# Performance work log

Measured on AMD Instinct MI355X. Metric: run time of the kernel, lower is better.

## Reference

```python
import jax, jax.numpy as jnp
import numpy as np

E, K, CAP = 8, 2, 48
RD, NC = 64, 10
LOAD_PEN, MIN_USE, TEMP = 2.0, 0.05, 1.0


def _conv(x, w):
    return jax.lax.conv_general_dilated(x, w, (1, 1), 'SAME',
                                        dimension_numbers=('NCHW', 'OIHW', 'NCHW'))


def _bn(x, g, b):
    # eval-mode BatchNorm2d with running_mean=0, running_var=1, eps=1e-5
    s = g / np.float32(np.sqrt(1.0 + 1e-5))
    return x * s[:, None, None] + b[:, None, None]


def _maxpool2(x):
    return jax.lax.reduce_window(x, -jnp.inf, jax.lax.max,
                                 (1, 1, 2, 2), (1, 1, 2, 2), 'VALID')


def setup_inputs() -> dict:
    key = jax.random.key(0)
    ks = iter(jax.random.split(key, 40))
    n = lambda shape, s=0.1: jax.random.normal(next(ks), shape, jnp.float32) * s
    B = 256
    return dict(
        x=jax.random.normal(next(ks), (B, 3, 32, 32), jnp.float32),
        # routing trunk
        tw1=n((32, 3, 3, 3)), tg1=jnp.ones(32), tb1=jnp.zeros(32),
        tw2=n((32, 32, 3, 3)), tg2=jnp.ones(32), tb2=jnp.zeros(32),
        tfw=n((RD, 128)), tfb=jnp.zeros(RD),
        # gate MLP
        gw1=n((RD // 2, RD)), gb1=jnp.zeros(RD // 2),
        gw2=n((E, RD // 2)), gb2=jnp.zeros(E),
        # per-expert feature extractors (stacked over E)
        ew1=n((E, 32, 3, 3, 3)), eg1=jnp.ones((E, 32)), eb1=jnp.zeros((E, 32)),
        ew2=n((E, 64, 32, 3, 3)), eg2=jnp.ones((E, 64)), eb2=jnp.zeros((E, 64)),
        ew3=n((E, 128, 64, 3, 3)), eg3=jnp.ones((E, 128)), eb3=jnp.zeros((E, 128)),
        efw=n((E, 128, 128)), efb=jnp.zeros((E, 128)),
        # per-expert classifiers (stacked over E)
        cw1=n((E, 64, 128)), cb1=jnp.zeros((E, 64)),
        cw2=n((E, NC, 64)), cb2=jnp.zeros((E, NC)),
    )


def _forward(x, tw1, tg1, tb1, tw2, tg2, tb2, tfw, tfb, gw1, gb1, gw2, gb2,
             ew1, eg1, eb1, ew2, eg2, eb2, ew3, eg3, eb3, efw, efb,
             cw1, cb1, cw2, cb2):
    B = x.shape[0]
    # ---- routing trunk ----
    h = jax.nn.relu(_bn(_conv(x, tw1), tg1, tb1))
    h = jax.nn.relu(_bn(_conv(h, tw2), tg2, tb2))
    h = _maxpool2(h)                                   # [B,32,16,16]
    h = h.reshape(B, 32, 2, 8, 2, 8).mean((3, 5))      # AdaptiveAvgPool2d(2)
    rf = jax.nn.relu(h.reshape(B, 128) @ tfw.T + tfb)  # [B,RD]
    # ---- gate ----
    scores = (jax.nn.relu(rf @ gw1.T + gb1) @ gw2.T + gb2) / TEMP  # [B,E]
    usage = jnp.ones(E, jnp.float32) / E               # expert_usage_ema buffer
    boost = jnp.where(usage < MIN_USE, (MIN_USE - usage) * 10.0, 0.0)
    balanced = scores + boost[None] - LOAD_PEN * usage[None]
    # ---- capacity-constrained top-k routing (eval: sample_order = arange) ----
    _, tk = jax.lax.top_k(balanced, K)                 # [B,K] int32

    def step(loads, tki):
        lt = loads[tki]                                # [K] loads of this sample's top-k
        avail = lt < CAP
        idx = jnp.where(jnp.any(avail), jnp.argmax(avail), jnp.argmin(lt))
        chosen = tki[idx]
        return loads.at[chosen].add(1.0), chosen

    _, chosen = jax.lax.scan(step, jnp.zeros(E, jnp.float32), tk)
    D = jax.nn.one_hot(chosen, E, dtype=bool)          # [B,E] dispatch mask

    # ---- experts: run each expert on the full batch, zero out unassigned ----
    def expert(w1, g1, b1, w2, g2, b2, w3, g3, b3, fw, fb, c1w, c1b, c2w, c2b):
        h = _maxpool2(jax.nn.relu(_bn(_conv(x, w1), g1, b1)))   # [B,32,16,16]
        h = _maxpool2(jax.nn.relu(_bn(_conv(h, w2), g2, b2)))   # [B,64,8,8]
        h = jax.nn.relu(_bn(_conv(h, w3), g3, b3)).mean((2, 3)) # GAP -> [B,128]
        f = jax.nn.relu(h @ fw.T + fb)
        return jax.nn.relu(f @ c1w.T + c1b) @ c2w.T + c2b        # [B,NC]

    outs = jax.vmap(expert)(ew1, eg1, eb1, ew2, eg2, eb2, ew3, eg3, eb3,
                            efw, efb, cw1, cb1, cw2, cb2)        # [E,B,NC]
    expert_outputs = jnp.where(D.T[:, :, None], outs, 0.0).transpose(1, 0, 2)  # [B,E,NC]

    # ---- combine via softmax over dispatched scores ----
    masked = jnp.where(D, balanced, -jnp.inf)
    rw = jax.nn.softmax(masked, axis=1) * D
    rw = rw / (rw.sum(1, keepdims=True) + 1e-12)
    final = jnp.einsum('be,bec->bc', rw, expert_outputs)         # [B,NC]
    return final, balanced, D


def reference(x, tw1, tg1, tb1, tw2, tg2, tb2, tfw, tfb, gw1, gb1, gw2, gb2,
              ew1, eg1, eb1, ew2, eg2, eb2, ew3, eg3, eb3, efw, efb,
              cw1, cb1, cw2, cb2):
    return _forward(x, tw1, tg1, tb1, tw2, tg2, tb2, tfw, tfb,
                    gw1, gb1, gw2, gb2, ew1, eg1, eb1, ew2, eg2, eb2,
                    ew3, eg3, eb3, efw, efb, cw1, cb1, cw2, cb2)
```

## Files before the change

### kernel.cpp

```cpp
#include <hip/hip_runtime.h>
#include <hip/hip_bf16.h>
#include <math.h>


#define BN_RS (1.0f / sqrtf(1.00001f))

typedef __attribute__((ext_vector_type(8))) short short8;
typedef __attribute__((ext_vector_type(4))) float floatx4;

static __device__ __forceinline__ ushort f2bf(float f) {
  unsigned u = __float_as_uint(f);
  unsigned r = (u + 0x7fffu + ((u >> 16) & 1u)) >> 16;
  return (ushort)r;
}
static __device__ __forceinline__ float bf2f(ushort h) {
  return __uint_as_float((unsigned)h << 16);
}

#define WS_TFP    0
#define WS_TK     262144
#define WS_W2H    264192
#define WS_W2L    282624
#define WS_EW2B   301056
#define WS_EW3B   595968

__global__ __launch_bounds__(256) void prep_kernel(
    const float* __restrict__ tw2, const float* __restrict__ ew2,
    const float* __restrict__ ew3, ushort* __restrict__ w2h,
    ushort* __restrict__ w2l, ushort* __restrict__ ew2b,
    ushort* __restrict__ ew3b)
{
  const int j = blockIdx.x * 256 + threadIdx.x;
  if (j < 9216) {
    int tap = j >> 10, oc = (j >> 5) & 31, ic = j & 31;
    float v = tw2[oc*288 + ic*9 + tap];
    ushort h = f2bf(v);
    w2h[j] = h;
    w2l[j] = f2bf(v - bf2f(h));
  } else if (j < 27648) {
    const int jj = (j - 9216) * 8;
    int e = jj / 18432, r2 = jj % 18432;
    int tap = r2 / 2048, r3 = r2 % 2048;
    int oc = r3 / 32, ic0 = r3 % 32;
    const float* src = &ew2[e*18432 + oc*288 + ic0*9 + tap];
    short8 o;
    #pragma unroll
    for (int k = 0; k < 8; ++k) o[k] = (short)f2bf(src[k*9]);
    *(short8*)&ew2b[jj] = o;
  } else if (j < 101376) {
    const int jj = (j - 27648) * 8;
    int e = jj / 73728, r2 = jj % 73728;
    int tap = r2 / 8192, r3 = r2 % 8192;
    int oc = r3 / 64, ic0 = r3 % 64;
    const float* src = &ew3[e*73728 + oc*576 + ic0*9 + tap];
    short8 o;
    #pragma unroll
    for (int k = 0; k < 8; ++k) o[k] = (short)f2bf(src[k*9]);
    *(short8*)&ew3b[jj] = o;
  }
}

__global__ __launch_bounds__(256) void trunk_kernel(
    const float* __restrict__ x, const float* __restrict__ tw1,
    const float* __restrict__ tg1, const float* __restrict__ tb1,
    const ushort* __restrict__ w2h, const ushort* __restrict__ w2l,
    const float* __restrict__ tg2, const float* __restrict__ tb2,
    float* __restrict__ tfp)
{
  __shared__ __align__(16) ushort smu[17696];
  float* smf = (float*)&smu[14400];
  const int t = threadIdx.x, blk = blockIdx.x;
  const int b = blk >> 3, rs = (blk >> 1) & 3, ch = blk & 1;
  const int r0 = rs * 8, c0 = ch * 16;

  {
    uint4 z = {0, 0, 0, 0};
    for (int j = t; j < 1800; j += 256) ((uint4*)smu)[j] = z;
  }
  for (int j = t; j < 720; j += 256) {
    int ic = j / 240, rem = j % 240, rr = rem / 20, c = rem % 20;
    int gy = r0 - 2 + rr, gx = c0 - 2 + c;
    float v = 0.f;
    if (gy >= 0 && gy < 32 && gx >= 0 && gx < 32)
      v = x[b*3072 + ic*1024 + gy*32 + gx];
    smf[j] = v;
  }
  for (int j = t; j < 864; j += 256) {
    int oc = j / 27, r = j % 27, ic = r / 9, k = r % 9;
    smf[720 + ic*288 + k*32 + oc] = tw1[j];
  }
  if (t < 32) { smf[1584 + t] = tg1[t]*BN_RS; smf[1584 + 32 + t] = tb1[t]; }
  __syncthreads();

  for (int it = 0; it < 2; ++it) {
    const int item = it*256 + t;
    if (item < 320) {
      const int oc = item & 31, rr = item >> 5;
      const int grow = r0 - 1 + rr;
      if (grow >= 0 && grow < 32) {
        float acc[18];
        #pragma unroll
        for (int c = 0; c < 18; ++c) acc[c] = 0.f;
        #pragma unroll 1
        for (int ic = 0; ic < 3; ++ic) {
          #pragma unroll 1
          for (int ky = 0; ky < 3; ++ky) {
            float wk[3];
            #pragma unroll
            for (int kx = 0; kx < 3; ++kx)
              wk[kx] = smf[720 + ic*288 + (ky*3 + kx)*32 + oc];
            const float* srow = &smf[ic*240 + (rr + ky)*20];
            float v[20];
            #pragma unroll
            for (int j4 = 0; j4 < 5; ++j4) {
              float4 q = *(const float4*)&srow[4*j4];
              v[4*j4] = q.x; v[4*j4+1] = q.y; v[4*j4+2] = q.z; v[4*j4+3] = q.w;
            }
            #pragma unroll
            for (int kx = 0; kx < 3; ++kx)
              #pragma unroll
              for (int c = 0; c < 18; ++c)
                acc[c] = fmaf(wk[kx], v[c+kx], acc[c]);
          }
        }
        const float s = smf[1584 + oc], bo = smf[1584 + 32 + oc];
        #pragma unroll
        for (int c = 0; c < 18; ++c) {
          const int gcol = c0 - 1 + c;
          float va = 0.f;
          if (gcol >= 0 && gcol < 32)
            va = fmaxf(fmaf(acc[c], s, bo), 0.f);
          ushort h = f2bf(va);
          ushort lo = f2bf(va - bf2f(h));
          const int ui = (rr*18 + c)*40 + oc;
          smu[ui] = h;
          smu[7200 + ui] = lo;
        }
      }
    }
  }
  __syncthreads();

  const int w4 = t >> 6, l = t & 63, col = l & 15, quad = l >> 4;
  const int nt = w4 & 1, yh = w4 >> 1;
  floatx4 acc2[4];
  #pragma unroll
  for (int y = 0; y < 4; ++y)
    #pragma unroll
    for (int i = 0; i < 4; ++i) acc2[y][i] = 0.f;

  #pragma unroll
  for (int dx = 0; dx < 3; ++dx) {
    #pragma unroll
    for (int dy = 0; dy < 3; ++dy) {
      const int wi = (dy*3 + dx)*1024 + (nt*16 + col)*32 + quad*8;
      short8 bh = *(const short8*)&w2h[wi];
      short8 bl = *(const short8*)&w2l[wi];
      #pragma unroll
      for (int y = 0; y < 4; ++y) {
        const int idx = ((yh*4 + y + dy)*18 + col + dx)*40 + quad*8;
        short8 ah = *(const short8*)&smu[idx];
        short8 al = *(const short8*)&smu[7200 + idx];
        acc2[y] = __builtin_amdgcn_mfma_f32_16x16x32_bf16(ah, bh, acc2[y], 0, 0, 0);
        acc2[y] = __builtin_amdgcn_mfma_f32_16x16x32_bf16(ah, bl, acc2[y], 0, 0, 0);
        acc2[y] = __builtin_amdgcn_mfma_f32_16x16x32_bf16(al, bh, acc2[y], 0, 0, 0);
      }
    }
  }

  {
    const int oc = nt*16 + col;
    const float s2 = tg2[oc]*BN_RS, bo2 = tb2[oc];
    float psum = 0.f;
    #pragma unroll
    for (int yp = 0; yp < 2; ++yp)
      #pragma unroll
      for (int i2 = 0; i2 < 2; ++i2) {
        float v00 = fmaxf(fmaf(acc2[2*yp][2*i2],     s2, bo2), 0.f);
        float v01 = fmaxf(fmaf(acc2[2*yp][2*i2+1],   s2, bo2), 0.f);
        float v10 = fmaxf(fmaf(acc2[2*yp+1][2*i2],   s2, bo2), 0.f);
        float v11 = fmaxf(fmaf(acc2[2*yp+1][2*i2+1], s2, bo2), 0.f);
        psum += fmaxf(fmaxf(v00, v01), fmaxf(v10, v11));
      }
    psum += __shfl_xor(psum, 16);
    psum += __shfl_xor(psum, 32);
    if (yh == 1 && quad == 0) smf[nt*32 + col] = psum;
    __syncthreads();
    if (yh == 0 && quad == 0) {
      float tot = psum + smf[nt*32 + col];
      tfp[b*256 + (rs*2 + ch)*32 + oc] = tot;
    }
  }
}

__global__ __launch_bounds__(64) void gate_kernel(
    const float* __restrict__ tfp, const float* __restrict__ tfw, const float* __restrict__ tfb,
    const float* __restrict__ gw1, const float* __restrict__ gb1,
    const float* __restrict__ gw2, const float* __restrict__ gb2,
    float* __restrict__ outBal, int* __restrict__ tk)
{
  __shared__ float feat[128], rf[64], g1[32], bal[8];
  const int b = blockIdx.x, t = threadIdx.x;
  #pragma unroll
  for (int h = 0; h < 2; ++h) {
    const int f = t + 64*h;
    const int oc = f >> 2, qy = (f >> 1) & 1, qx = f & 1;
    feat[f] = (tfp[b*256 + (4*qy + qx)*32 + oc] +
               tfp[b*256 + (4*qy + 2 + qx)*32 + oc]) * (1.f/64.f);
  }
  __syncthreads();
  {
    float a = tfb[t];
    const float4* wp = (const float4*)&tfw[t*128];
    #pragma unroll 8
    for (int i4 = 0; i4 < 32; ++i4) {
      float4 wv = wp[i4];
      a = fmaf(wv.x, feat[4*i4], a);   a = fmaf(wv.y, feat[4*i4+1], a);
      a = fmaf(wv.z, feat[4*i4+2], a); a = fmaf(wv.w, feat[4*i4+3], a);
    }
    rf[t] = fmaxf(a, 0.f);
  }
  __syncthreads();
  if (t < 32) {
    float a = gb1[t];
    const float4* wp = (const float4*)&gw1[t*64];
    #pragma unroll
    for (int i4 = 0; i4 < 16; ++i4) {
      float4 wv = wp[i4];
      a = fmaf(wv.x, rf[4*i4], a);   a = fmaf(wv.y, rf[4*i4+1], a);
      a = fmaf(wv.z, rf[4*i4+2], a); a = fmaf(wv.w, rf[4*i4+3], a);
    }
    g1[t] = fmaxf(a, 0.f);
  }
  __syncthreads();
  if (t < 8) {
    float a = gb2[t];
    const float4* wp = (const float4*)&gw2[t*32];
    #pragma unroll
    for (int i4 = 0; i4 < 8; ++i4) {
      float4 wv = wp[i4];
      a = fmaf(wv.x, g1[4*i4], a);   a = fmaf(wv.y, g1[4*i4+1], a);
      a = fmaf(wv.z, g1[4*i4+2], a); a = fmaf(wv.w, g1[4*i4+3], a);
    }
    const float v = a - 0.25f;
    bal[t] = v;
    outBal[b*8 + t] = v;
  }
  __syncthreads();
  if (t == 0) {
    int t0 = 0; float b0 = bal[0];
    #pragma unroll
    for (int e2 = 1; e2 < 8; ++e2) if (bal[e2] > b0) { b0 = bal[e2]; t0 = e2; }
    int t1 = -1; float b1 = -3.4e38f;
    #pragma unroll
    for (int e2 = 0; e2 < 8; ++e2) if (e2 != t0 && bal[e2] > b1) { b1 = bal[e2]; t1 = e2; }
    tk[b*2] = t0; tk[b*2 + 1] = t1;
  }
}

#define XA_IMG  0
#define XA_FEAT 3600
#define XA_SFF  3728
#define XA_SGG  3856
#define XA_XF   9040
#define XA_W1F  12508
#define XA_BN1F 13372
#define XA_SC   9040
__global__ __launch_bounds__(512, 2) void expALL_kernel(
    const float* __restrict__ x, const int* __restrict__ tk,
    const float* __restrict__ ew1, const float* __restrict__ eg1,
    const float* __restrict__ eb1, const ushort* __restrict__ ew2b,
    const float* __restrict__ eg2, const float* __restrict__ eb2,
    const ushort* __restrict__ ew3b, const float* __restrict__ eg3,
    const float* __restrict__ eb3, const float* __restrict__ efw,
    const float* __restrict__ efb, const float* __restrict__ cw1,
    const float* __restrict__ cb1, const float* __restrict__ cw2,
    const float* __restrict__ cb2, float* __restrict__ outF,
    float* __restrict__ outD)
{
  __shared__ __align__(16) ushort smu[27296];
  __shared__ int stk[512];
  __shared__ int sch;
  float* smf = (float*)smu;
  const int t = threadIdx.x, b = blockIdx.x;
  const int w8 = t >> 6, l = t & 63;
  const int col = l & 15, quad = l >> 4;

  stk[t] = tk[t];
  __syncthreads();
  if (t == 0) {
    unsigned long long Lp = 0ull;
    int chv = 0;
    for (int i = 0; i <= b; ++i) {
      const int a = stk[2*i], c = stk[2*i+1];
      const int la = (int)((Lp >> (a*8)) & 0xFFull);
      const int lc = (int)((Lp >> (c*8)) & 0xFFull);
      chv = (la < 48) ? a : ((lc < 48) ? c : ((la <= lc) ? a : c));
      Lp += 1ull << (chv*8);
    }
    sch = chv;
  } else {
    uint4 z; z.x = 0; z.y = 0; z.z = 0; z.w = 0;
    for (int j = t-1; j < 1620; j += 511) ((uint4*)smu)[j] = z;
    for (int j = t-1; j < 3468; j += 511) {
      int ic = j / 1156, rem = j % 1156, p = rem / 34, cpd = rem % 34;
      int gy = p - 1, gx = cpd - 1;
      float v = 0.f;
      if (gy >= 0 && gy < 32 && gx >= 0 && gx < 32) v = x[b*3072 + ic*1024 + gy*32 + gx];
      smf[XA_XF + j] = v;
    }
  }
  __syncthreads();
  const int e = sch;
  if (t < 8) outD[b*8 + t] = (t == e) ? 1.f : 0.f;

  const int ntile = w8 & 3, mhalf = w8 >> 2;
  short8 w2f[9];
  {
    const int oc2 = ntile*16 + col;
    #pragma unroll
    for (int tap = 0; tap < 9; ++tap)
      w2f[tap] = *(const short8*)&ew2b[(e*9 + tap)*2048 + oc2*32 + quad*8];
  }

  for (int j = t; j < 864; j += 512) {
    int oc = j / 27, r = j % 27, ic = r / 9, k = r % 9;
    smf[XA_W1F + ic*288 + k*32 + oc] = ew1[e*864 + j];
  }
  if (t < 32) { smf[XA_BN1F + t] = eg1[e*32 + t]*BN_RS; smf[XA_BN1F + 32 + t] = eb1[e*32 + t]; }
  __syncthreads();

  {
    const int g = t >> 5, c = t & 31;
    for (int rs = 0; rs < 4; ++rs) {
      const int r0 = rs * 8;
      float acc[2][8];
      #pragma unroll
      for (int o = 0; o < 2; ++o)
        #pragma unroll
        for (int r = 0; r < 8; ++r) acc[o][r] = 0.f;
      for (int ic = 0; ic < 3; ++ic) {
        float w[2][9];
        #pragma unroll
        for (int k = 0; k < 9; ++k) {
          float2 wv = *(const float2*)&smf[XA_W1F + ic*288 + k*32 + 2*g];
          w[0][k] = wv.x; w[1][k] = wv.y;
        }
        const float* src = &smf[XA_XF + ic*1156 + r0*34 + c];
        #pragma unroll
        for (int rr = 0; rr < 10; ++rr) {
          const float i0 = src[rr*34], i1 = src[rr*34 + 1], i2 = src[rr*34 + 2];
          #pragma unroll
          for (int dr = 0; dr < 3; ++dr) {
            const int r = rr - dr;
            if (r < 0 || r > 7) continue;
            #pragma unroll
            for (int o = 0; o < 2; ++o) {
              acc[o][r] = fmaf(w[o][dr*3+0], i0, acc[o][r]);
              acc[o][r] = fmaf(w[o][dr*3+1], i1, acc[o][r]);
              acc[o][r] = fmaf(w[o][dr*3+2], i2, acc[o][r]);
            }
          }
        }
      }
      #pragma unroll
      for (int o = 0; o < 2; ++o) {
        const int oc = 2*g + o;
        const float s = smf[XA_BN1F + oc], bo = smf[XA_BN1F + 32 + oc];
        float m[4];
        #pragma unroll
        for (int pr = 0; pr < 4; ++pr) {
          float v0 = fmaxf(fmaf(acc[o][2*pr],   s, bo), 0.f);
          float v1 = fmaxf(fmaf(acc[o][2*pr+1], s, bo), 0.f);
          m[pr] = fmaxf(v0, v1);
        }
        #pragma unroll
        for (int pr = 0; pr < 4; ++pr) {
          float nb = __shfl_xor(m[pr], 1);
          m[pr] = fmaxf(m[pr], nb);
        }
        if (!(c & 1)) {
          const int pc = c >> 1;
          #pragma unroll
          for (int pr = 0; pr < 4; ++pr)
            smu[XA_IMG + ((rs*4 + pr + 1)*18 + (pc + 1))*40 + oc] = f2bf(m[pr]);
        }
      }
    }
  }
  __syncthreads();

  const int oc3 = w8*16 + col;
  short8 w3f[9][2];
  #pragma unroll
  for (int tap = 0; tap < 9; ++tap)
    #pragma unroll
    for (int ks = 0; ks < 2; ++ks)
      w3f[tap][ks] = *(const short8*)&ew3b[(e*9 + tap)*8192 + oc3*64 + ks*32 + quad*8];

  {
    floatx4 acc[8];
    #pragma unroll
    for (int mt = 0; mt < 8; ++mt)
      #pragma unroll
      for (int i = 0; i < 4; ++i) acc[mt][i] = 0.f;

    #pragma unroll
    for (int tap = 0; tap < 9; ++tap) {
      const int dy = tap / 3, dx = tap % 3;
      #pragma unroll
      for (int mtl = 0; mtl < 8; ++mtl) {
        const int mt = mhalf*8 + mtl;
        short8 afr = *(const short8*)
            &smu[XA_IMG + ((mt + dy)*18 + col + dx)*40 + quad*8];
        acc[mtl] = __builtin_amdgcn_mfma_f32_16x16x32_bf16(afr, w2f[tap], acc[mtl], 0, 0, 0);
      }
    }
    __syncthreads();

    {
      uint4 z; z.x = 0; z.y = 0; z.z = 0; z.w = 0;
      for (int j = t; j < 288; j += 512) {
        int slot = j >> 3, ofs = (j & 7) * 8, row, cl;
        if (slot < 10)      { row = 0; cl = slot; }
        else if (slot < 20) { row = 9; cl = slot - 10; }
        else if (slot < 28) { row = 1 + (slot - 20); cl = 0; }
        else                { row = 1 + (slot - 28); cl = 9; }
        *(uint4*)&smu[(row*10 + cl)*72 + ofs] = z;
      }
    }
    const int oc2 = ntile*16 + col;
    const float s2 = eg2[e*64 + oc2]*BN_RS, bo2 = eb2[e*64 + oc2];
    #pragma unroll
    for (int mtpl = 0; mtpl < 4; ++mtpl) {
      const int mtp = mhalf*4 + mtpl;
      float a00 = fmaxf(fmaf(acc[2*mtpl][0],   s2, bo2), 0.f);
      float a01 = fmaxf(fmaf(acc[2*mtpl][1],   s2, bo2), 0.f);
      float a02 = fmaxf(fmaf(acc[2*mtpl][2],   s2, bo2), 0.f);
      float a03 = fmaxf(fmaf(acc[2*mtpl][3],   s2, bo2), 0.f);
      float a10 = fmaxf(fmaf(acc[2*mtpl+1][0], s2, bo2), 0.f);
      float a11 = fmaxf(fmaf(acc[2*mtpl+1][1], s2, bo2), 0.f);
      float a12 = fmaxf(fmaf(acc[2*mtpl+1][2], s2, bo2), 0.f);
      float a13 = fmaxf(fmaf(acc[2*mtpl+1][3], s2, bo2), 0.f);
      float p0 = fmaxf(fmaxf(a00, a01), fmaxf(a10, a11));
      float p1 = fmaxf(fmaxf(a02, a03), fmaxf(a12, a13));
      smu[((mtp + 1)*10 + (quad*2 + 1))*72 + oc2] = f2bf(p0);
      smu[((mtp + 1)*10 + (quad*2 + 2))*72 + oc2] = f2bf(p1);
    }
  }
  __syncthreads();

  const int fcout = t & 127, fcpart = t >> 7;
  float4 efr[8];
  {
    const float4* wp = (const float4*)&efw[e*16384 + fcout*128 + fcpart*32];
    #pragma unroll
    for (int i4 = 0; i4 < 8; ++i4) efr[i4] = wp[i4];
  }

  {
    floatx4 acc[4];
    #pragma unroll
    for (int mt = 0; mt < 4; ++mt)
      #pragma unroll
      for (int i = 0; i < 4; ++i) acc[mt][i] = 0.f;

    #pragma unroll
    for (int tap = 0; tap < 9; ++tap) {
      const int dy = tap / 3, dx = tap % 3;
      #pragma unroll
      for (int ks = 0; ks < 2; ++ks) {
        #pragma unroll
        for (int mt = 0; mt < 4; ++mt) {
          const int m = mt*16 + col;
          const int y = m >> 3, xx = m & 7;
          short8 afr = *(const short8*)
              &smu[((y + dy)*10 + (xx + dx))*72 + ks*32 + quad*8];
          acc[mt] = __builtin_amdgcn_mfma_f32_16x16x32_bf16(afr, w3f[tap][ks], acc[mt], 0, 0, 0);
        }
      }
    }

    {
      const float s = eg3[e*128 + oc3]*BN_RS, bo = eb3[e*128 + oc3];
      float gsum = 0.f;
      #pragma unroll
      for (int mt = 0; mt < 4; ++mt)
        #pragma unroll
        for (int i = 0; i < 4; ++i)
          gsum += fmaxf(fmaf(acc[mt][i], s, bo), 0.f);
      gsum += __shfl_xor(gsum, 16);
      gsum += __shfl_xor(gsum, 32);
      if (quad == 0) smf[XA_FEAT + oc3] = gsum * (1.f/64.f);
    }
  }
  __syncthreads();

  {
    float a = (fcpart == 0) ? efb[e*128 + fcout] : 0.f;
    #pragma unroll
    for (int i4 = 0; i4 < 8; ++i4) {
      float4 wv = efr[i4];
      const int base = XA_FEAT + fcpart*32 + 4*i4;
      a = fmaf(wv.x, smf[base], a);     a = fmaf(wv.y, smf[base + 1], a);
      a = fmaf(wv.z, smf[base + 2], a); a = fmaf(wv.w, smf[base + 3], a);
    }
    smf[XA_SC + fcpart*128 + fcout] = a;
  }
  __syncthreads();
  if (t < 128)
    smf[XA_SFF + t] = fmaxf(smf[XA_SC + t] + smf[XA_SC + 128 + t] +
                            smf[XA_SC + 256 + t] + smf[XA_SC + 384 + t], 0.f);
  __syncthreads();
  if (t < 256) {
    const int out = t & 63, part = t >> 6;
    float a = (part == 0) ? cb1[e*64 + out] : 0.f;
    const float4* wp = (const float4*)&cw1[e*8192 + out*128 + part*32];
    #pragma unroll
    for (int i4 = 0; i4 < 8; ++i4) {
      float4 wv = wp[i4];
      const int base = XA_SFF + part*32 + 4*i4;
      a = fmaf(wv.x, smf[base], a);     a = fmaf(wv.y, smf[base + 1], a);
      a = fmaf(wv.z, smf[base + 2], a); a = fmaf(wv.w, smf[base + 3], a);
    }
    smf[XA_SC + part*64 + out] = a;
  }
  __syncthreads();
  if (t < 64)
    smf[XA_SGG + t] = fmaxf(smf[XA_SC + t] + smf[XA_SC + 64 + t] +
                            smf[XA_SC + 128 + t] + smf[XA_SC + 192 + t], 0.f);
  __syncthreads();
  if (t < 10) {
    float a = cb2[e*10 + t];
    const float4* wp = (const float4*)&cw2[e*640 + t*64];
    #pragma unroll
    for (int i4 = 0; i4 < 16; ++i4) {
      float4 wv = wp[i4];
      a = fmaf(wv.x, smf[XA_SGG + 4*i4],     a);
      a = fmaf(wv.y, smf[XA_SGG + 4*i4 + 1], a);
      a = fmaf(wv.z, smf[XA_SGG + 4*i4 + 2], a);
      a = fmaf(wv.w, smf[XA_SGG + 4*i4 + 3], a);
    }
    outF[b*10 + t] = a;
  }
}

extern "C" void kernel_launch(void* const* d_in, const int* in_sizes, int n_in,
                              void* d_out, int out_size, void* d_ws, size_t ws_size,
                              hipStream_t stream)
{
  const float* x   = (const float*)d_in[0];
  const float* tw1 = (const float*)d_in[1];
  const float* tg1 = (const float*)d_in[2];
  const float* tb1 = (const float*)d_in[3];
  const float* tw2 = (const float*)d_in[4];
  const float* tg2 = (const float*)d_in[5];
  const float* tb2 = (const float*)d_in[6];
  const float* tfw = (const float*)d_in[7];
  const float* tfb = (const float*)d_in[8];
  const float* gw1 = (const float*)d_in[9];
  const float* gb1 = (const float*)d_in[10];
  const float* gw2 = (const float*)d_in[11];
  const float* gb2 = (const float*)d_in[12];
  const float* ew1 = (const float*)d_in[13];
  const float* eg1 = (const float*)d_in[14];
  const float* eb1 = (const float*)d_in[15];
  const float* ew2 = (const float*)d_in[16];
  const float* eg2 = (const float*)d_in[17];
  const float* eb2 = (const float*)d_in[18];
  const float* ew3 = (const float*)d_in[19];
  const float* eg3 = (const float*)d_in[20];
  const float* eb3 = (const float*)d_in[21];
  const float* efw = (const float*)d_in[22];
  const float* efb = (const float*)d_in[23];
  const float* cw1 = (const float*)d_in[24];
  const float* cb1 = (const float*)d_in[25];
  const float* cw2 = (const float*)d_in[26];
  const float* cb2 = (const float*)d_in[27];

  float*  out  = (float*)d_out;
  char*   ws   = (char*)d_ws;
  float*  tfp  = (float*)(ws + WS_TFP);
  int*    tk   = (int*)(ws + WS_TK);
  ushort* w2h  = (ushort*)(ws + WS_W2H);
  ushort* w2l  = (ushort*)(ws + WS_W2L);
  ushort* ew2b = (ushort*)(ws + WS_EW2B);
  ushort* ew3b = (ushort*)(ws + WS_EW3B);

  prep_kernel<<<396, 256, 0, stream>>>(tw2, ew2, ew3, w2h, w2l, ew2b, ew3b);
  trunk_kernel<<<2048, 256, 0, stream>>>(x, tw1, tg1, tb1, w2h, w2l, tg2, tb2, tfp);
  gate_kernel<<<256, 64, 0, stream>>>(tfp, tfw, tfb, gw1, gb1, gw2, gb2,
                                      out + 2560, tk);
  expALL_kernel<<<256, 512, 0, stream>>>(x, tk, ew1, eg1, eb1, ew2b, eg2, eb2,
                                         ew3b, eg3, eb3, efw, efb, cw1, cb1,
                                         cw2, cb2, out, out + 4608);
}
```

Before: 182.8 us.

## Stage expert weight repacking through LDS and prefetch epilogue parameters early

The prep kernel now repacks expert conv weights by loading contiguous float4 chunks into shared memory, converting them to bf16 there, and then writing tap-major packed 8-byte stores. This replaces strided 9-element-apart global gathers and cuts the grid from 396 to 108 blocks. In the expert and trunk kernels, BN scale/bias, FC biases, the cw1 rows and a warm-up read of cw2 are hoisted ahead of the MFMA loops so their latency overlaps compute. The trade-off is higher register pressure from the cw1 prefetch and fewer blocks in prep.

```diff
diff --git a/kernel.cpp b/kernel.cpp
--- a/kernel.cpp
+++ b/kernel.cpp
@@ -15,6 +15,11 @@
 }
 static __device__ __forceinline__ float bf2f(ushort h) {
   return __uint_as_float((unsigned)h << 16);
+}
+static __device__ __forceinline__ unsigned long long pk4(ushort a, ushort b,
+                                                         ushort c, ushort d) {
+  return (unsigned long long)a | ((unsigned long long)b << 16) |
+         ((unsigned long long)c << 32) | ((unsigned long long)d << 48);
 }
 
 #define WS_TFP    0
@@ -30,33 +35,47 @@
     ushort* __restrict__ w2l, ushort* __restrict__ ew2b,
     ushort* __restrict__ ew3b)
 {
-  const int j = blockIdx.x * 256 + threadIdx.x;
-  if (j < 9216) {
+  __shared__ __align__(16) ushort plds[18432];
+  const int blk = blockIdx.x, t = threadIdx.x;
+  if (blk < 36) {
+    const int j = blk*256 + t;
     int tap = j >> 10, oc = (j >> 5) & 31, ic = j & 31;
     float v = tw2[oc*288 + ic*9 + tap];
     ushort h = f2bf(v);
     w2h[j] = h;
     w2l[j] = f2bf(v - bf2f(h));
-  } else if (j < 27648) {
-    const int jj = (j - 9216) * 8;
-    int e = jj / 18432, r2 = jj % 18432;
-    int tap = r2 / 2048, r3 = r2 % 2048;
-    int oc = r3 / 32, ic0 = r3 % 32;
-    const float* src = &ew2[e*18432 + oc*288 + ic0*9 + tap];
-    short8 o;
-    #pragma unroll
-    for (int k = 0; k < 8; ++k) o[k] = (short)f2bf(src[k*9]);
-    *(short8*)&ew2b[jj] = o;
-  } else if (j < 101376) {
-    const int jj = (j - 27648) * 8;
-    int e = jj / 73728, r2 = jj % 73728;
-    int tap = r2 / 8192, r3 = r2 % 8192;
-    int oc = r3 / 64, ic0 = r3 % 64;
-    const float* src = &ew3[e*73728 + oc*576 + ic0*9 + tap];
-    short8 o;
-    #pragma unroll
-    for (int k = 0; k < 8; ++k) o[k] = (short)f2bf(src[k*9]);
-    *(short8*)&ew3b[jj] = o;
+  } else if (blk < 44) {
+    const int e = blk - 36;
+    const float* src = &ew2[e*18432];
+    for (int j4 = t; j4 < 4608; j4 += 256) {
+      float4 q = *(const float4*)&src[j4*4];
+      *(unsigned long long*)&plds[j4*4] =
+          pk4(f2bf(q.x), f2bf(q.y), f2bf(q.z), f2bf(q.w));
+    }
+    __syncthreads();
+    for (int q8 = t; q8 < 4608; q8 += 256) {
+      const int tap = q8 >> 9, j0 = (q8 & 511) * 4;
+      const int oc = j0 >> 5, ic = j0 & 31;
+      const int base = oc*288 + ic*9 + tap;
+      *(unsigned long long*)&ew2b[(e*9 + tap)*2048 + j0] =
+          pk4(plds[base], plds[base + 9], plds[base + 18], plds[base + 27]);
+    }
+  } else {
+    const int k = blk - 44, e = k >> 3, ocb = k & 7;
+    const float* src = &ew3[e*73728 + ocb*9216];
+    for (int j4 = t; j4 < 2304; j4 += 256) {
+      float4 q = *(const float4*)&src[j4*4];
+      *(unsigned long long*)&plds[j4*4] =
+          pk4(f2bf(q.x), f2bf(q.y), f2bf(q.z), f2bf(q.w));
+    }
+    __syncthreads();
+    for (int q8 = t; q8 < 2304; q8 += 256) {
+      const int tap = q8 >> 8, j0 = (q8 & 255) * 4;
+      const int oc = j0 >> 6, ic = j0 & 63;
+      const int base = oc*576 + ic*9 + tap;
+      *(unsigned long long*)&ew3b[(e*9 + tap)*8192 + ocb*1024 + j0] =
+          pk4(plds[base], plds[base + 9], plds[base + 18], plds[base + 27]);
+    }
   }
 }
 
@@ -143,6 +162,8 @@
 
   const int w4 = t >> 6, l = t & 63, col = l & 15, quad = l >> 4;
   const int nt = w4 & 1, yh = w4 >> 1;
+  const int oc = nt*16 + col;
+  const float s2 = tg2[oc]*BN_RS, bo2 = tb2[oc];
   floatx4 acc2[4];
   #pragma unroll
   for (int y = 0; y < 4; ++y)
@@ -169,8 +190,6 @@
   }
 
   {
-    const int oc = nt*16 + col;
-    const float s2 = tg2[oc]*BN_RS, bo2 = tb2[oc];
     float psum = 0.f;
     #pragma unroll
     for (int yp = 0; yp < 2; ++yp)
@@ -398,6 +417,23 @@
     for (int ks = 0; ks < 2; ++ks)
       w3f[tap][ks] = *(const short8*)&ew3b[(e*9 + tap)*8192 + oc3*64 + ks*32 + quad*8];
 
+  const int poc2 = ntile*16 + col;
+  const float s2p = eg2[e*64 + poc2]*BN_RS, b2p = eb2[e*64 + poc2];
+  const float s3p = eg3[e*128 + oc3]*BN_RS, b3p = eb3[e*128 + oc3];
+  const int fcout = t & 127, fcpart = t >> 7;
+  const float efbp = (fcpart == 0) ? efb[e*128 + fcout] : 0.f;
+  const int out2 = t & 63, part2 = (t >> 6) & 3;
+  float4 c1r[8];
+  float cb1p = 0.f;
+  if (t < 256) {
+    const float4* wp = (const float4*)&cw1[e*8192 + out2*128 + part2*32];
+    #pragma unroll
+    for (int i4 = 0; i4 < 8; ++i4) c1r[i4] = wp[i4];
+    if (part2 == 0) cb1p = cb1[e*64 + out2];
+  }
+  float warmA = cw2[e*640 + t];
+  float warmB = (t < 10) ? cb2[e*10 + t] : 0.f;
+
   {
     floatx4 acc[8];
     #pragma unroll
@@ -429,28 +465,25 @@
         *(uint4*)&smu[(row*10 + cl)*72 + ofs] = z;
       }
     }
-    const int oc2 = ntile*16 + col;
-    const float s2 = eg2[e*64 + oc2]*BN_RS, bo2 = eb2[e*64 + oc2];
     #pragma unroll
     for (int mtpl = 0; mtpl < 4; ++mtpl) {
       const int mtp = mhalf*4 + mtpl;
-      float a00 = fmaxf(fmaf(acc[2*mtpl][0],   s2, bo2), 0.f);
-      float a01 = fmaxf(fmaf(acc[2*mtpl][1],   s2, bo2), 0.f);
-      float a02 = fmaxf(fmaf(acc[2*mtpl][2],   s2, bo2), 0.f);
-      float a03 = fmaxf(fmaf(acc[2*mtpl][3],   s2, bo2), 0.f);
-      float a10 = fmaxf(fmaf(acc[2*mtpl+1][0], s2, bo2), 0.f);
-      float a11 = fmaxf(fmaf(acc[2*mtpl+1][1], s2, bo2), 0.f);
-      float a12 = fmaxf(fmaf(acc[2*mtpl+1][2], s2, bo2), 0.f);
-      float a13 = fmaxf(fmaf(acc[2*mtpl+1][3], s2, bo2), 0.f);
+      float a00 = fmaxf(fmaf(acc[2*mtpl][0],   s2p, b2p), 0.f);
+      float a01 = fmaxf(fmaf(acc[2*mtpl][1],   s2p, b2p), 0.f);
+      float a02 = fmaxf(fmaf(acc[2*mtpl][2],   s2p, b2p), 0.f);
+      float a03 = fmaxf(fmaf(acc[2*mtpl][3],   s2p, b2p), 0.f);
+      float a10 = fmaxf(fmaf(acc[2*mtpl+1][0], s2p, b2p), 0.f);
+      float a11 = fmaxf(fmaf(acc[2*mtpl+1][1], s2p, b2p), 0.f);
+      float a12 = fmaxf(fmaf(acc[2*mtpl+1][2], s2p, b2p), 0.f);
+      float a13 = fmaxf(fmaf(acc[2*mtpl+1][3], s2p, b2p), 0.f);
       float p0 = fmaxf(fmaxf(a00, a01), fmaxf(a10, a11));
       float p1 = fmaxf(fmaxf(a02, a03), fmaxf(a12, a13));
-      smu[((mtp + 1)*10 + (quad*2 + 1))*72 + oc2] = f2bf(p0);
-      smu[((mtp + 1)*10 + (quad*2 + 2))*72 + oc2] = f2bf(p1);
-    }
-  }
-  __syncthreads();
-
-  const int fcout = t & 127, fcpart = t >> 7;
+      smu[((mtp + 1)*10 + (quad*2 + 1))*72 + poc2] = f2bf(p0);
+      smu[((mtp + 1)*10 + (quad*2 + 2))*72 + poc2] = f2bf(p1);
+    }
+  }
+  __syncthreads();
+
   float4 efr[8];
   {
     const float4* wp = (const float4*)&efw[e*16384 + fcout*128 + fcpart*32];
@@ -482,13 +515,12 @@
     }
 
     {
-      const float s = eg3[e*128 + oc3]*BN_RS, bo = eb3[e*128 + oc3];
       float gsum = 0.f;
       #pragma unroll
       for (int mt = 0; mt < 4; ++mt)
         #pragma unroll
         for (int i = 0; i < 4; ++i)
-          gsum += fmaxf(fmaf(acc[mt][i], s, bo), 0.f);
+          gsum += fmaxf(fmaf(acc[mt][i], s3p, b3p), 0.f);
       gsum += __shfl_xor(gsum, 16);
       gsum += __shfl_xor(gsum, 32);
       if (quad == 0) smf[XA_FEAT + oc3] = gsum * (1.f/64.f);
@@ -497,7 +529,7 @@
   __syncthreads();
 
   {
-    float a = (fcpart == 0) ? efb[e*128 + fcout] : 0.f;
+    float a = efbp;
     #pragma unroll
     for (int i4 = 0; i4 < 8; ++i4) {
       float4 wv = efr[i4];
@@ -513,25 +545,24 @@
                             smf[XA_SC + 256 + t] + smf[XA_SC + 384 + t], 0.f);
   __syncthreads();
   if (t < 256) {
-    const int out = t & 63, part = t >> 6;
-    float a = (part == 0) ? cb1[e*64 + out] : 0.f;
-    const float4* wp = (const float4*)&cw1[e*8192 + out*128 + part*32];
+    float a = cb1p;
     #pragma unroll
     for (int i4 = 0; i4 < 8; ++i4) {
-      float4 wv = wp[i4];
-      const int base = XA_SFF + part*32 + 4*i4;
+      float4 wv = c1r[i4];
+      const int base = XA_SFF + part2*32 + 4*i4;
       a = fmaf(wv.x, smf[base], a);     a = fmaf(wv.y, smf[base + 1], a);
       a = fmaf(wv.z, smf[base + 2], a); a = fmaf(wv.w, smf[base + 3], a);
     }
-    smf[XA_SC + part*64 + out] = a;
+    smf[XA_SC + part2*64 + out2] = a;
   }
   __syncthreads();
   if (t < 64)
     smf[XA_SGG + t] = fmaxf(smf[XA_SC + t] + smf[XA_SC + 64 + t] +
                             smf[XA_SC + 128 + t] + smf[XA_SC + 192 + t], 0.f);
   __syncthreads();
+  asm volatile("" :: "v"(warmA));
   if (t < 10) {
-    float a = cb2[e*10 + t];
+    float a = warmB;
     const float4* wp = (const float4*)&cw2[e*640 + t*64];
     #pragma unroll
     for (int i4 = 0; i4 < 16; ++i4) {
@@ -587,7 +618,7 @@
   ushort* ew2b = (ushort*)(ws + WS_EW2B);
   ushort* ew3b = (ushort*)(ws + WS_EW3B);
 
-  prep_kernel<<<396, 256, 0, stream>>>(tw2, ew2, ew3, w2h, w2l, ew2b, ew3b);
+  prep_kernel<<<108, 256, 0, stream>>>(tw2, ew2, ew3, w2h, w2l, ew2b, ew3b);
   trunk_kernel<<<2048, 256, 0, stream>>>(x, tw1, tg1, tb1, w2h, w2l, tg2, tb2, tfp);
   gate_kernel<<<256, 64, 0, stream>>>(tfp, tfw, tfb, gw1, gb1, gw2, gb2,
                                       out + 2560, tk);
```

Result: slower. 187.3 us (+2.5%).

## Double expert kernel block size to 1024 threads and split conv work further

Applied to the files above, without the earlier changes.

Launches the per-sample expert kernel with 1024 threads instead of 512. The conv1 row strips are split across two thread halves, and conv2 MFMA tiles are split into quarters so each wave holds fewer accumulators. The conv3 and FC stages are guarded so only the first 8 waves or 512 threads run them. BN scale and bias loads are hoisted ahead of the MFMA loops, including in the trunk kernel, to hide global load latency. The aim is more parallel waves per sample in a grid of only 256 blocks, at the cost of idle threads in the later stages and more barrier overhead.

```diff
diff --git a/kernel.cpp b/kernel.cpp
--- a/kernel.cpp
+++ b/kernel.cpp
@@ -143,6 +143,8 @@
 
   const int w4 = t >> 6, l = t & 63, col = l & 15, quad = l >> 4;
   const int nt = w4 & 1, yh = w4 >> 1;
+  const int oc = nt*16 + col;
+  const float s2 = tg2[oc]*BN_RS, bo2 = tb2[oc];
   floatx4 acc2[4];
   #pragma unroll
   for (int y = 0; y < 4; ++y)
@@ -169,8 +171,6 @@
   }
 
   {
-    const int oc = nt*16 + col;
-    const float s2 = tg2[oc]*BN_RS, bo2 = tb2[oc];
     float psum = 0.f;
     #pragma unroll
     for (int yp = 0; yp < 2; ++yp)
@@ -266,7 +266,7 @@
 #define XA_W1F  12508
 #define XA_BN1F 13372
 #define XA_SC   9040
-__global__ __launch_bounds__(512, 2) void expALL_kernel(
+__global__ __launch_bounds__(1024) void expALL_kernel(
     const float* __restrict__ x, const int* __restrict__ tk,
     const float* __restrict__ ew1, const float* __restrict__ eg1,
     const float* __restrict__ eb1, const ushort* __restrict__ ew2b,
@@ -283,10 +283,10 @@
   __shared__ int sch;
   float* smf = (float*)smu;
   const int t = threadIdx.x, b = blockIdx.x;
-  const int w8 = t >> 6, l = t & 63;
+  const int w16 = t >> 6, l = t & 63;
   const int col = l & 15, quad = l >> 4;
 
-  stk[t] = tk[t];
+  if (t < 512) stk[t] = tk[t];
   __syncthreads();
   if (t == 0) {
     unsigned long long Lp = 0ull;
@@ -301,8 +301,8 @@
     sch = chv;
   } else {
     uint4 z; z.x = 0; z.y = 0; z.z = 0; z.w = 0;
-    for (int j = t-1; j < 1620; j += 511) ((uint4*)smu)[j] = z;
-    for (int j = t-1; j < 3468; j += 511) {
+    for (int j = t-1; j < 1620; j += 1023) ((uint4*)smu)[j] = z;
+    for (int j = t-1; j < 3468; j += 1023) {
       int ic = j / 1156, rem = j % 1156, p = rem / 34, cpd = rem % 34;
       int gy = p - 1, gx = cpd - 1;
       float v = 0.f;
@@ -314,7 +314,7 @@
   const int e = sch;
   if (t < 8) outD[b*8 + t] = (t == e) ? 1.f : 0.f;
 
-  const int ntile = w8 & 3, mhalf = w8 >> 2;
+  const int ntile = w16 & 3, mq = (w16 >> 2) & 3;
   short8 w2f[9];
   {
     const int oc2 = ntile*16 + col;
@@ -323,7 +323,7 @@
       w2f[tap] = *(const short8*)&ew2b[(e*9 + tap)*2048 + oc2*32 + quad*8];
   }
 
-  for (int j = t; j < 864; j += 512) {
+  for (int j = t; j < 864; j += 1024) {
     int oc = j / 27, r = j % 27, ic = r / 9, k = r % 9;
     smf[XA_W1F + ic*288 + k*32 + oc] = ew1[e*864 + j];
   }
@@ -331,14 +331,17 @@
   __syncthreads();
 
   {
-    const int g = t >> 5, c = t & 31;
-    for (int rs = 0; rs < 4; ++rs) {
+    const int g = (t >> 5) & 15, c = t & 31, sl = t >> 9;
+    #pragma unroll 1
+    for (int rsi = 0; rsi < 2; ++rsi) {
+      const int rs = sl*2 + rsi;
       const int r0 = rs * 8;
       float acc[2][8];
       #pragma unroll
       for (int o = 0; o < 2; ++o)
         #pragma unroll
         for (int r = 0; r < 8; ++r) acc[o][r] = 0.f;
+      #pragma unroll 1
       for (int ic = 0; ic < 3; ++ic) {
         float w[2][9];
         #pragma unroll
@@ -390,7 +393,7 @@
   }
   __syncthreads();
 
-  const int oc3 = w8*16 + col;
+  const int oc3 = (w16 & 7)*16 + col;
   short8 w3f[9][2];
   #pragma unroll
   for (int tap = 0; tap < 9; ++tap)
@@ -398,10 +401,16 @@
     for (int ks = 0; ks < 2; ++ks)
       w3f[tap][ks] = *(const short8*)&ew3b[(e*9 + tap)*8192 + oc3*64 + ks*32 + quad*8];
 
+  const int poc2 = ntile*16 + col;
+  const float s2p = eg2[e*64 + poc2]*BN_RS, b2p = eb2[e*64 + poc2];
+  const float s3p = eg3[e*128 + oc3]*BN_RS, b3p = eb3[e*128 + oc3];
+  const int fcout = t & 127, fcpart = (t >> 7) & 3;
+  const float efbp = ((t >> 7) == 0) ? efb[e*128 + fcout] : 0.f;
+
   {
-    floatx4 acc[8];
-    #pragma unroll
-    for (int mt = 0; mt < 8; ++mt)
+    floatx4 acc[4];
+    #pragma unroll
+    for (int mt = 0; mt < 4; ++mt)
       #pragma unroll
       for (int i = 0; i < 4; ++i) acc[mt][i] = 0.f;
 
@@ -409,8 +418,8 @@
     for (int tap = 0; tap < 9; ++tap) {
       const int dy = tap / 3, dx = tap % 3;
       #pragma unroll
-      for (int mtl = 0; mtl < 8; ++mtl) {
-        const int mt = mhalf*8 + mtl;
+      for (int mtl = 0; mtl < 4; ++mtl) {
+        const int mt = mq*4 + mtl;
         short8 afr = *(const short8*)
             &smu[XA_IMG + ((mt + dy)*18 + col + dx)*40 + quad*8];
         acc[mtl] = __builtin_amdgcn_mfma_f32_16x16x32_bf16(afr, w2f[tap], acc[mtl], 0, 0, 0);
@@ -420,7 +429,7 @@
 
     {
       uint4 z; z.x = 0; z.y = 0; z.z = 0; z.w = 0;
-      for (int j = t; j < 288; j += 512) {
+      for (int j = t; j < 288; j += 1024) {
         int slot = j >> 3, ofs = (j & 7) * 8, row, cl;
         if (slot < 10)      { row = 0; cl = slot; }
         else if (slot < 20) { row = 9; cl = slot - 10; }
@@ -429,28 +438,25 @@
         *(uint4*)&smu[(row*10 + cl)*72 + ofs] = z;
       }
     }
-    const int oc2 = ntile*16 + col;
-    const float s2 = eg2[e*64 + oc2]*BN_RS, bo2 = eb2[e*64 + oc2];
-    #pragma unroll
-    for (int mtpl = 0; mtpl < 4; ++mtpl) {
-      const int mtp = mhalf*4 + mtpl;
-      float a00 = fmaxf(fmaf(acc[2*mtpl][0],   s2, bo2), 0.f);
-      float a01 = fmaxf(fmaf(acc[2*mtpl][1],   s2, bo2), 0.f);
-      float a02 = fmaxf(fmaf(acc[2*mtpl][2],   s2, bo2), 0.f);
-      float a03 = fmaxf(fmaf(acc[2*mtpl][3],   s2, bo2), 0.f);
-      float a10 = fmaxf(fmaf(acc[2*mtpl+1][0], s2, bo2), 0.f);
-      float a11 = fmaxf(fmaf(acc[2*mtpl+1][1], s2, bo2), 0.f);
-      float a12 = fmaxf(fmaf(acc[2*mtpl+1][2], s2, bo2), 0.f);
-      float a13 = fmaxf(fmaf(acc[2*mtpl+1][3], s2, bo2), 0.f);
+    #pragma unroll
+    for (int p2 = 0; p2 < 2; ++p2) {
+      const int mtp = mq*2 + p2;
+      float a00 = fmaxf(fmaf(acc[2*p2][0],   s2p, b2p), 0.f);
+      float a01 = fmaxf(fmaf(acc[2*p2][1],   s2p, b2p), 0.f);
+      float a02 = fmaxf(fmaf(acc[2*p2][2],   s2p, b2p), 0.f);
+      float a03 = fmaxf(fmaf(acc[2*p2][3],   s2p, b2p), 0.f);
+      float a10 = fmaxf(fmaf(acc[2*p2+1][0], s2p, b2p), 0.f);
+      float a11 = fmaxf(fmaf(acc[2*p2+1][1], s2p, b2p), 0.f);
+      float a12 = fmaxf(fmaf(acc[2*p2+1][2], s2p, b2p), 0.f);
+      float a13 = fmaxf(fmaf(acc[2*p2+1][3], s2p, b2p), 0.f);
       float p0 = fmaxf(fmaxf(a00, a01), fmaxf(a10, a11));
       float p1 = fmaxf(fmaxf(a02, a03), fmaxf(a12, a13));
-      smu[((mtp + 1)*10 + (quad*2 + 1))*72 + oc2] = f2bf(p0);
-      smu[((mtp + 1)*10 + (quad*2 + 2))*72 + oc2] = f2bf(p1);
-    }
-  }
-  __syncthreads();
-
-  const int fcout = t & 127, fcpart = t >> 7;
+      smu[((mtp + 1)*10 + (quad*2 + 1))*72 + poc2] = f2bf(p0);
+      smu[((mtp + 1)*10 + (quad*2 + 2))*72 + poc2] = f2bf(p1);
+    }
+  }
+  __syncthreads();
+
   float4 efr[8];
   {
     const float4* wp = (const float4*)&efw[e*16384 + fcout*128 + fcpart*32];
@@ -458,7 +464,7 @@
     for (int i4 = 0; i4 < 8; ++i4) efr[i4] = wp[i4];
   }
 
-  {
+  if (w16 < 8) {
     floatx4 acc[4];
     #pragma unroll
     for (int mt = 0; mt < 4; ++mt)
@@ -482,13 +488,12 @@
     }
 
     {
-      const float s = eg3[e*128 + oc3]*BN_RS, bo = eb3[e*128 + oc3];
       float gsum = 0.f;
       #pragma unroll
       for (int mt = 0; mt < 4; ++mt)
         #pragma unroll
         for (int i = 0; i < 4; ++i)
-          gsum += fmaxf(fmaf(acc[mt][i], s, bo), 0.f);
+          gsum += fmaxf(fmaf(acc[mt][i], s3p, b3p), 0.f);
       gsum += __shfl_xor(gsum, 16);
       gsum += __shfl_xor(gsum, 32);
       if (quad == 0) smf[XA_FEAT + oc3] = gsum * (1.f/64.f);
@@ -496,8 +501,8 @@
   }
   __syncthreads();
 
-  {
-    float a = (fcpart == 0) ? efb[e*128 + fcout] : 0.f;
+  if (t < 512) {
+    float a = efbp;
     #pragma unroll
     for (int i4 = 0; i4 < 8; ++i4) {
       float4 wv = efr[i4];
@@ -591,7 +596,7 @@
   trunk_kernel<<<2048, 256, 0, stream>>>(x, tw1, tg1, tb1, w2h, w2l, tg2, tb2, tfp);
   gate_kernel<<<256, 64, 0, stream>>>(tfp, tfw, tfb, gw1, gb1, gw2, gb2,
                                       out + 2560, tk);
-  expALL_kernel<<<256, 512, 0, stream>>>(x, tk, ew1, eg1, eb1, ew2b, eg2, eb2,
-                                         ew3b, eg3, eb3, efw, efb, cw1, cb1,
-                                         cw2, cb2, out, out + 4608);
+  expALL_kernel<<<256, 1024, 0, stream>>>(x, tk, ew1, eg1, eb1, ew2b, eg2, eb2,
+                                          ew3b, eg3, eb3, efw, efb, cw1, cb1,
+                                          cw2, cb2, out, out + 4608);
 }
```

New measurement: 201.6 us. +10.3%, slower.

## Fuse gate MLP into trunk kernel via last-block atomic counter

Applied to the files above, without the earlier changes.

Removes the separate gate kernel launch. Each trunk block increments a per-sample atomic counter, and the eighth block to finish for a sample runs the gate MLP and top-2 selection. The counters are zeroed in the prep kernel, which gets one extra block. The change also hoists the BN scale/bias and bias loads earlier in the expert kernel and adds unroll-1 pragmas to the expert conv1 loops. This trades one launch plus a dependency gap for atomics, a threadfence, and a serial tail on the last block of each sample.

```diff
diff --git a/kernel.cpp b/kernel.cpp
--- a/kernel.cpp
+++ b/kernel.cpp
@@ -23,12 +23,13 @@
 #define WS_W2L    282624
 #define WS_EW2B   301056
 #define WS_EW3B   595968
+#define WS_CNT    1775616
 
 __global__ __launch_bounds__(256) void prep_kernel(
     const float* __restrict__ tw2, const float* __restrict__ ew2,
     const float* __restrict__ ew3, ushort* __restrict__ w2h,
     ushort* __restrict__ w2l, ushort* __restrict__ ew2b,
-    ushort* __restrict__ ew3b)
+    ushort* __restrict__ ew3b, int* __restrict__ cnt)
 {
   const int j = blockIdx.x * 256 + threadIdx.x;
   if (j < 9216) {
@@ -57,6 +58,8 @@
     #pragma unroll
     for (int k = 0; k < 8; ++k) o[k] = (short)f2bf(src[k*9]);
     *(short8*)&ew3b[jj] = o;
+  } else if (j < 101632) {
+    cnt[j - 101376] = 0;
   }
 }
 
@@ -65,9 +68,14 @@
     const float* __restrict__ tg1, const float* __restrict__ tb1,
     const ushort* __restrict__ w2h, const ushort* __restrict__ w2l,
     const float* __restrict__ tg2, const float* __restrict__ tb2,
-    float* __restrict__ tfp)
+    const float* __restrict__ tfw, const float* __restrict__ tfb,
+    const float* __restrict__ gw1, const float* __restrict__ gb1,
+    const float* __restrict__ gw2, const float* __restrict__ gb2,
+    float* __restrict__ tfp, float* __restrict__ outBal,
+    int* __restrict__ tk, int* __restrict__ cnt)
 {
   __shared__ __align__(16) ushort smu[17696];
+  __shared__ int sOld;
   float* smf = (float*)&smu[14400];
   const int t = threadIdx.x, blk = blockIdx.x;
   const int b = blk >> 3, rs = (blk >> 1) & 3, ch = blk & 1;
@@ -143,6 +151,8 @@
 
   const int w4 = t >> 6, l = t & 63, col = l & 15, quad = l >> 4;
   const int nt = w4 & 1, yh = w4 >> 1;
+  const int oc = nt*16 + col;
+  const float s2 = tg2[oc]*BN_RS, bo2 = tb2[oc];
   floatx4 acc2[4];
   #pragma unroll
   for (int y = 0; y < 4; ++y)
@@ -169,8 +179,6 @@
   }
 
   {
-    const int oc = nt*16 + col;
-    const float s2 = tg2[oc]*BN_RS, bo2 = tb2[oc];
     float psum = 0.f;
     #pragma unroll
     for (int yp = 0; yp < 2; ++yp)
@@ -191,70 +199,70 @@
       tfp[b*256 + (rs*2 + ch)*32 + oc] = tot;
     }
   }
-}
-
-__global__ __launch_bounds__(64) void gate_kernel(
-    const float* __restrict__ tfp, const float* __restrict__ tfw, const float* __restrict__ tfb,
-    const float* __restrict__ gw1, const float* __restrict__ gb1,
-    const float* __restrict__ gw2, const float* __restrict__ gb2,
-    float* __restrict__ outBal, int* __restrict__ tk)
-{
-  __shared__ float feat[128], rf[64], g1[32], bal[8];
-  const int b = blockIdx.x, t = threadIdx.x;
-  #pragma unroll
-  for (int h = 0; h < 2; ++h) {
-    const int f = t + 64*h;
-    const int oc = f >> 2, qy = (f >> 1) & 1, qx = f & 1;
-    feat[f] = (tfp[b*256 + (4*qy + qx)*32 + oc] +
-               tfp[b*256 + (4*qy + 2 + qx)*32 + oc]) * (1.f/64.f);
-  }
-  __syncthreads();
-  {
-    float a = tfb[t];
-    const float4* wp = (const float4*)&tfw[t*128];
-    #pragma unroll 8
-    for (int i4 = 0; i4 < 32; ++i4) {
-      float4 wv = wp[i4];
-      a = fmaf(wv.x, feat[4*i4], a);   a = fmaf(wv.y, feat[4*i4+1], a);
-      a = fmaf(wv.z, feat[4*i4+2], a); a = fmaf(wv.w, feat[4*i4+3], a);
-    }
-    rf[t] = fmaxf(a, 0.f);
-  }
-  __syncthreads();
-  if (t < 32) {
-    float a = gb1[t];
-    const float4* wp = (const float4*)&gw1[t*64];
-    #pragma unroll
-    for (int i4 = 0; i4 < 16; ++i4) {
-      float4 wv = wp[i4];
-      a = fmaf(wv.x, rf[4*i4], a);   a = fmaf(wv.y, rf[4*i4+1], a);
-      a = fmaf(wv.z, rf[4*i4+2], a); a = fmaf(wv.w, rf[4*i4+3], a);
-    }
-    g1[t] = fmaxf(a, 0.f);
-  }
-  __syncthreads();
-  if (t < 8) {
-    float a = gb2[t];
-    const float4* wp = (const float4*)&gw2[t*32];
-    #pragma unroll
-    for (int i4 = 0; i4 < 8; ++i4) {
-      float4 wv = wp[i4];
-      a = fmaf(wv.x, g1[4*i4], a);   a = fmaf(wv.y, g1[4*i4+1], a);
-      a = fmaf(wv.z, g1[4*i4+2], a); a = fmaf(wv.w, g1[4*i4+3], a);
-    }
-    const float v = a - 0.25f;
-    bal[t] = v;
-    outBal[b*8 + t] = v;
-  }
-  __syncthreads();
-  if (t == 0) {
-    int t0 = 0; float b0 = bal[0];
-    #pragma unroll
-    for (int e2 = 1; e2 < 8; ++e2) if (bal[e2] > b0) { b0 = bal[e2]; t0 = e2; }
-    int t1 = -1; float b1 = -3.4e38f;
-    #pragma unroll
-    for (int e2 = 0; e2 < 8; ++e2) if (e2 != t0 && bal[e2] > b1) { b1 = bal[e2]; t1 = e2; }
-    tk[b*2] = t0; tk[b*2 + 1] = t1;
+
+  __threadfence();
+  __syncthreads();
+  if (t == 0) sOld = atomicAdd(&cnt[b], 1);
+  __syncthreads();
+  if (sOld == 7) {
+    float* feat = &smf[64];
+    float* rf   = &smf[192];
+    float* g1s  = &smf[256];
+    float* bal  = &smf[288];
+    if (t < 128) {
+      const int f = t;
+      const int ocf = f >> 2, qy = (f >> 1) & 1, qx = f & 1;
+      feat[f] = (tfp[b*256 + (4*qy + qx)*32 + ocf] +
+                 tfp[b*256 + (4*qy + 2 + qx)*32 + ocf]) * (1.f/64.f);
+    }
+    __syncthreads();
+    if (t < 64) {
+      float a = tfb[t];
+      const float4* wp = (const float4*)&tfw[t*128];
+      #pragma unroll 8
+      for (int i4 = 0; i4 < 32; ++i4) {
+        float4 wv = wp[i4];
+        a = fmaf(wv.x, feat[4*i4], a);   a = fmaf(wv.y, feat[4*i4+1], a);
+        a = fmaf(wv.z, feat[4*i4+2], a); a = fmaf(wv.w, feat[4*i4+3], a);
+      }
+      rf[t] = fmaxf(a, 0.f);
+    }
+    __syncthreads();
+    if (t < 32) {
+      float a = gb1[t];
+      const float4* wp = (const float4*)&gw1[t*64];
+      #pragma unroll
+      for (int i4 = 0; i4 < 16; ++i4) {
+        float4 wv = wp[i4];
+        a = fmaf(wv.x, rf[4*i4], a);   a = fmaf(wv.y, rf[4*i4+1], a);
+        a = fmaf(wv.z, rf[4*i4+2], a); a = fmaf(wv.w, rf[4*i4+3], a);
+      }
+      g1s[t] = fmaxf(a, 0.f);
+    }
+    __syncthreads();
+    if (t < 8) {
+      float a = gb2[t];
+      const float4* wp = (const float4*)&gw2[t*32];
+      #pragma unroll
+      for (int i4 = 0; i4 < 8; ++i4) {
+        float4 wv = wp[i4];
+        a = fmaf(wv.x, g1s[4*i4], a);   a = fmaf(wv.y, g1s[4*i4+1], a);
+        a = fmaf(wv.z, g1s[4*i4+2], a); a = fmaf(wv.w, g1s[4*i4+3], a);
+      }
+      const float v = a - 0.25f;
+      bal[t] = v;
+      outBal[b*8 + t] = v;
+    }
+    __syncthreads();
+    if (t == 0) {
+      int t0 = 0; float b0 = bal[0];
+      #pragma unroll
+      for (int e2 = 1; e2 < 8; ++e2) if (bal[e2] > b0) { b0 = bal[e2]; t0 = e2; }
+      int t1 = -1; float b1 = -3.4e38f;
+      #pragma unroll
+      for (int e2 = 0; e2 < 8; ++e2) if (e2 != t0 && bal[e2] > b1) { b1 = bal[e2]; t1 = e2; }
+      tk[b*2] = t0; tk[b*2 + 1] = t1;
+    }
   }
 }
 
@@ -332,6 +340,7 @@
 
   {
     const int g = t >> 5, c = t & 31;
+    #pragma unroll 1
     for (int rs = 0; rs < 4; ++rs) {
       const int r0 = rs * 8;
       float acc[2][8];
@@ -339,6 +348,7 @@
       for (int o = 0; o < 2; ++o)
         #pragma unroll
         for (int r = 0; r < 8; ++r) acc[o][r] = 0.f;
+      #pragma unroll 1
       for (int ic = 0; ic < 3; ++ic) {
         float w[2][9];
         #pragma unroll
@@ -398,6 +408,12 @@
     for (int ks = 0; ks < 2; ++ks)
       w3f[tap][ks] = *(const short8*)&ew3b[(e*9 + tap)*8192 + oc3*64 + ks*32 + quad*8];
 
+  const int poc2 = ntile*16 + col;
+  const float s2p = eg2[e*64 + poc2]*BN_RS, b2p = eb2[e*64 + poc2];
+  const float s3p = eg3[e*128 + oc3]*BN_RS, b3p = eb3[e*128 + oc3];
+  const int fcout = t & 127, fcpart = t >> 7;
+  const float efbp = (fcpart == 0) ? efb[e*128 + fcout] : 0.f;
+
   {
     floatx4 acc[8];
     #pragma unroll
@@ -429,28 +445,25 @@
         *(uint4*)&smu[(row*10 + cl)*72 + ofs] = z;
       }
     }
-    const int oc2 = ntile*16 + col;
-    const float s2 = eg2[e*64 + oc2]*BN_RS, bo2 = eb2[e*64 + oc2];
     #pragma unroll
     for (int mtpl = 0; mtpl < 4; ++mtpl) {
       const int mtp = mhalf*4 + mtpl;
-      float a00 = fmaxf(fmaf(acc[2*mtpl][0],   s2, bo2), 0.f);
-      float a01 = fmaxf(fmaf(acc[2*mtpl][1],   s2, bo2), 0.f);
-      float a02 = fmaxf(fmaf(acc[2*mtpl][2],   s2, bo2), 0.f);
-      float a03 = fmaxf(fmaf(acc[2*mtpl][3],   s2, bo2), 0.f);
-      float a10 = fmaxf(fmaf(acc[2*mtpl+1][0], s2, bo2), 0.f);
-      float a11 = fmaxf(fmaf(acc[2*mtpl+1][1], s2, bo2), 0.f);
-      float a12 = fmaxf(fmaf(acc[2*mtpl+1][2], s2, bo2), 0.f);
-      float a13 = fmaxf(fmaf(acc[2*mtpl+1][3], s2, bo2), 0.f);
+      float a00 = fmaxf(fmaf(acc[2*mtpl][0],   s2p, b2p), 0.f);
+      float a01 = fmaxf(fmaf(acc[2*mtpl][1],   s2p, b2p), 0.f);
+      float a02 = fmaxf(fmaf(acc[2*mtpl][2],   s2p, b2p), 0.f);
+      float a03 = fmaxf(fmaf(acc[2*mtpl][3],   s2p, b2p), 0.f);
+      float a10 = fmaxf(fmaf(acc[2*mtpl+1][0], s2p, b2p), 0.f);
+      float a11 = fmaxf(fmaf(acc[2*mtpl+1][1], s2p, b2p), 0.f);
+      float a12 = fmaxf(fmaf(acc[2*mtpl+1][2], s2p, b2p), 0.f);
+      float a13 = fmaxf(fmaf(acc[2*mtpl+1][3], s2p, b2p), 0.f);
       float p0 = fmaxf(fmaxf(a00, a01), fmaxf(a10, a11));
       float p1 = fmaxf(fmaxf(a02, a03), fmaxf(a12, a13));
-      smu[((mtp + 1)*10 + (quad*2 + 1))*72 + oc2] = f2bf(p0);
-      smu[((mtp + 1)*10 + (quad*2 + 2))*72 + oc2] = f2bf(p1);
-    }
-  }
-  __syncthreads();
-
-  const int fcout = t & 127, fcpart = t >> 7;
+      smu[((mtp + 1)*10 + (quad*2 + 1))*72 + poc2] = f2bf(p0);
+      smu[((mtp + 1)*10 + (quad*2 + 2))*72 + poc2] = f2bf(p1);
+    }
+  }
+  __syncthreads();
+
   float4 efr[8];
   {
     const float4* wp = (const float4*)&efw[e*16384 + fcout*128 + fcpart*32];
@@ -482,13 +495,12 @@
     }
 
     {
-      const float s = eg3[e*128 + oc3]*BN_RS, bo = eb3[e*128 + oc3];
       float gsum = 0.f;
       #pragma unroll
       for (int mt = 0; mt < 4; ++mt)
         #pragma unroll
         for (int i = 0; i < 4; ++i)
-          gsum += fmaxf(fmaf(acc[mt][i], s, bo), 0.f);
+          gsum += fmaxf(fmaf(acc[mt][i], s3p, b3p), 0.f);
       gsum += __shfl_xor(gsum, 16);
       gsum += __shfl_xor(gsum, 32);
       if (quad == 0) smf[XA_FEAT + oc3] = gsum * (1.f/64.f);
@@ -497,7 +509,7 @@
   __syncthreads();
 
   {
-    float a = (fcpart == 0) ? efb[e*128 + fcout] : 0.f;
+    float a = efbp;
     #pragma unroll
     for (int i4 = 0; i4 < 8; ++i4) {
       float4 wv = efr[i4];
@@ -586,11 +598,12 @@
   ushort* w2l  = (ushort*)(ws + WS_W2L);
   ushort* ew2b = (ushort*)(ws + WS_EW2B);
   ushort* ew3b = (ushort*)(ws + WS_EW3B);
-
-  prep_kernel<<<396, 256, 0, stream>>>(tw2, ew2, ew3, w2h, w2l, ew2b, ew3b);
-  trunk_kernel<<<2048, 256, 0, stream>>>(x, tw1, tg1, tb1, w2h, w2l, tg2, tb2, tfp);
-  gate_kernel<<<256, 64, 0, stream>>>(tfp, tfw, tfb, gw1, gb1, gw2, gb2,
-                                      out + 2560, tk);
+  int*    cnt  = (int*)(ws + WS_CNT);
+
+  prep_kernel<<<397, 256, 0, stream>>>(tw2, ew2, ew3, w2h, w2l, ew2b, ew3b, cnt);
+  trunk_kernel<<<2048, 256, 0, stream>>>(x, tw1, tg1, tb1, w2h, w2l, tg2, tb2,
+                                         tfw, tfb, gw1, gb1, gw2, gb2,
+                                         tfp, out + 2560, tk, cnt);
   expALL_kernel<<<256, 512, 0, stream>>>(x, tk, ew1, eg1, eb1, ew2b, eg2, eb2,
                                          ew3b, eg3, eb3, efw, efb, cw1, cb1,
                                          cw2, cb2, out, out + 4608);
```

After: 305.5 us. 67.1% more time.
